# Performance work log

Hardware: AMD Instinct MI355X
Metric: run time of the kernel (lower is better)

The kernel has to match this reference:

```python
import jax, jax.numpy as jnp
import numpy as np

KSIZE = 7
NSPIX = 196


def _unfold(x, k):
    # x: (T, C, H, W) -> (T, C, k*k, H, W), reflect padding, torch Unfold ordering
    p = (k - 1) // 2
    T, C, H, W = x.shape
    xp = jnp.pad(x, ((0, 0), (0, 0), (p, p), (p, p)), mode='reflect')
    return jnp.stack([xp[:, :, i:i + H, j:j + W] for i in range(k) for j in range(k)], axis=2)


def setup_inputs() -> dict:
    key = jax.random.key(0)
    k1, k2, k3, k4, k5 = jax.random.split(key, 5)
    T, C, H, W = 2, 64, 160, 160
    fan_in = C * KSIZE * KSIZE
    x = jax.random.normal(k1, (T, C, H, W), jnp.float32)
    spix = jax.random.randint(k2, (T, H, W), 0, NSPIX, jnp.int32)
    W_lin = jax.random.normal(k3, (C, fan_in), jnp.float32) / np.sqrt(fan_in)
    b_lin = jax.random.normal(k4, (C,), jnp.float32) * 0.01
    w_scale = jax.random.normal(k5, (C,), jnp.float32) / np.sqrt(C)
    b_scale = jnp.zeros((1,), jnp.float32)
    return {"x": x, "spix": spix, "W_lin": W_lin, "b_lin": b_lin,
            "w_scale": w_scale, "b_scale": b_scale}


def reference(x, spix, W_lin, b_lin, w_scale, b_scale):
    T, C, H, W = x.shape
    K2 = KSIZE * KSIZE
    O = W_lin.shape[0]
    p = (KSIZE - 1) // 2

    # unfold(x) with reflect padding -> patches (T, C, K2, H, W)
    patches = _unfold(x, KSIZE)

    # unfold(spix) -> neighbor superpixel ids per pixel (T, K2, H, W)
    sp = jnp.pad(spix, ((0, 0), (p, p), (p, p)), mode='reflect')
    nb = jnp.stack([sp[:, i:i + H, j:j + W] for i in range(KSIZE) for j in range(KSIZE)], axis=1)

    # per-frame superpixel mean pooling (bist.get_pooled_video): down (T, S, C)
    seg = (spix.astype(jnp.int32) + jnp.arange(T, dtype=jnp.int32)[:, None, None] * NSPIX).reshape(-1)
    feats = x.transpose(0, 2, 3, 1).reshape(-1, C)  # (T*H*W, C)
    sums = jax.ops.segment_sum(feats, seg, num_segments=T * NSPIX).reshape(T, NSPIX, C)
    cnts = jax.ops.segment_sum(jnp.ones((seg.shape[0],), x.dtype), seg,
                               num_segments=T * NSPIX).reshape(T, NSPIX, 1)
    down = sums / jnp.maximum(cnts, 1.0)

    # squared pairwise distances between superpixel means: pwd (T, S, S)
    sq = jnp.sum(down * down, axis=-1)
    pwd = jnp.maximum(sq[:, :, None] + sq[:, None, :]
                      - 2.0 * jnp.einsum('tsc,tuc->tsu', down, down), 0.0)

    # sims[t,k,h,w] = ||mean(spix[t,h,w]) - mean(nb[t,k,h,w])||^2
    tidx = jnp.arange(T)[:, None, None, None]
    sims = pwd[tidx, spix[:, None, :, :], nb]  # (T, K2, H, W)

    # scale = 10 * softplus(1x1-conv(x / ||x||_c))  -> (T, H, W)
    xn = x / (jnp.linalg.norm(x, axis=1, keepdims=True) + 1e-10)
    scale = 10.0 * jax.nn.softplus(jnp.einsum('c,tchw->thw', w_scale, xn) + b_scale[0])

    # apply_norm 'exp_max' over the kernel-tap axis
    rw = jnp.exp(-scale[:, None, :, :] * sims)  # (T, K2, H, W)
    rw = rw / (1e-5 + jnp.max(rw, axis=1, keepdims=True))

    # dynamic conv: out[t,o,h,w] = sum_{c,k} W[o,c,k] * patches[t,c,k,h,w] * rw[t,k,h,w] + b[o]
    out = jnp.einsum('ock,tckhw,tkhw->tohw', W_lin.reshape(O, C, K2), patches, rw)
    return out + b_lin[None, :, None, None]
```

## Files before the change

kernel.cpp:

```cpp
#include <hip/hip_runtime.h>
#include <math.h>

#define TT 2
#define CC 64
#define HH 160
#define WW 160
#define KS 7
#define K2 49
#define NSPIX 196
#define HWSZ (HH*WW)
#define PAD 3
#define OO 64
#define FANIN (CC*K2)
#define TS 8
#define PS (TS+KS-1)
#define NPOS (PS*PS)

#define NCHUNK 50
#define CHUNKPIX 512

typedef _Float16 half8 __attribute__((ext_vector_type(8)));
typedef float f32x16 __attribute__((ext_vector_type(16)));
typedef unsigned int uint4v __attribute__((ext_vector_type(4)));
typedef _Float16 half2v __attribute__((ext_vector_type(2)));

__device__ __forceinline__ int reflect(int i, int n) {
    if (i < 0) i = -i;
    if (i >= n) i = 2*n - 2 - i;
    return i;
}

__global__ __launch_bounds__(256) void k_prep(const float* __restrict__ x,
                                              const int* __restrict__ spix,
                                              const float* __restrict__ Wl,
                                              const float* __restrict__ wsc,
                                              const float* __restrict__ bsc,
                                              float* __restrict__ sums,
                                              float* __restrict__ cnts,
                                              float* __restrict__ scale,
                                              _Float16* __restrict__ Wb,
                                              _Float16* __restrict__ xT) {
    __shared__ float ls[8*200];
    __shared__ float lcnt[200];
    int bid = blockIdx.x;
    int tid = threadIdx.x;

    if (bid < 800) {
        int cg = bid & 7;
        int rest = bid >> 3;
        int ch = rest % NCHUNK;
        int t  = rest / NCHUNK;

        for (int i = tid; i < 8*200; i += 256) ls[i] = 0.f;
        if (cg == 0) for (int i = tid; i < 200; i += 256) lcnt[i] = 0.f;
        __syncthreads();

        int base = ch*CHUNKPIX;
        const float* xb = x + ((size_t)t*CC + cg*8)*HWSZ;
        #pragma unroll
        for (int i = 0; i < CHUNKPIX; i += 256) {
            int pix = base + i + tid;
            int s = spix[t*HWSZ + pix];
            if (cg == 0) atomicAdd(&lcnt[s], 1.0f);
            #pragma unroll
            for (int j = 0; j < 8; ++j) atomicAdd(&ls[j*200 + s], xb[(size_t)j*HWSZ + pix]);
        }
        __syncthreads();

        float* sb = sums + (size_t)t*NSPIX*CC + cg*8;
        for (int i = tid; i < 8*NSPIX; i += 256) {
            int s = i >> 3, j = i & 7;
            float v = ls[j*200 + s];
            if (v != 0.f) atomicAdd(&sb[s*CC + j], v);
        }
        if (cg == 0)
            for (int i = tid; i < NSPIX; i += 256) {
                float v = lcnt[i];
                if (v != 0.f) atomicAdd(&cnts[t*NSPIX + i], v);
            }
    } else if (bid < 1000) {
        int pix = (bid - 800)*256 + tid;
        int t = pix / HWSZ, hw = pix - t*HWSZ;
        const float* xs = x + (size_t)t*CC*HWSZ + hw;
        float s1 = 0.f, s2 = 0.f;
        unsigned int pk[32];
        #pragma unroll
        for (int cp = 0; cp < 32; ++cp) {
            float v0 = xs[(size_t)(2*cp)*HWSZ];
            float v1 = xs[(size_t)(2*cp + 1)*HWSZ];
            s1 += wsc[2*cp]*v0 + wsc[2*cp+1]*v1;
            s2 = fmaf(v0, v0, s2); s2 = fmaf(v1, v1, s2);
            half2v h; h[0] = (_Float16)v0; h[1] = (_Float16)v1;
            pk[cp] = __builtin_bit_cast(unsigned int, h);
        }
        float z = s1/(sqrtf(s2) + 1e-10f) + bsc[0];
        float sp_ = (z > 0.f) ? z + log1pf(expf(-z)) : log1pf(expf(z));
        scale[pix] = 10.f*sp_;
        uint4v* dst = (uint4v*)(xT + (size_t)pix*64);
        #pragma unroll
        for (int q = 0; q < 8; ++q) {
            uint4v v = { pk[4*q], pk[4*q+1], pk[4*q+2], pk[4*q+3] };
            dst[q] = v;
        }
    } else {
        int row = (bid - 1000)*256 + tid;
        if (row < 2*K2*4*64) {
            int ln  = row & 63;
            int kc  = (row >> 6) & 3;
            int tq  = row >> 8;
            int tap = tq % K2;
            int qo  = tq / K2;
            int o = qo*32 + (ln & 31);
            int cb = kc*16 + (ln >> 5)*8;
            _Float16* dst = Wb + (size_t)row*8;
            const float* src = Wl + (size_t)o*FANIN + tap;
            #pragma unroll
            for (int j = 0; j < 8; ++j) dst[j] = (_Float16)src[(size_t)(cb + j)*K2];
        }
    }
}

__global__ __launch_bounds__(256) void k_pwd(const float* __restrict__ sums,
                                             const float* __restrict__ cnts,
                                             float* __restrict__ pwd) {
    int tid = blockIdx.x*256 + threadIdx.x;
    if (tid >= TT*NSPIX*NSPIX) return;
    int t = tid / (NSPIX*NSPIX); int r = tid - t*NSPIX*NSPIX;
    int s = r / NSPIX, u = r - (r / NSPIX)*NSPIX;
    const float* ds = sums + (size_t)(t*NSPIX + s)*CC;
    const float* du = sums + (size_t)(t*NSPIX + u)*CC;
    float is = 1.0f / fmaxf(cnts[t*NSPIX + s], 1.0f);
    float iu = 1.0f / fmaxf(cnts[t*NSPIX + u], 1.0f);
    float acc = 0.f;
    #pragma unroll 8
    for (int c = 0; c < CC; ++c) {
        float d = ds[c]*is - du[c]*iu;
        acc = fmaf(d, d, acc);
    }
    pwd[tid] = acc;
}

__global__ __launch_bounds__(256, 4) void k_main(
    const _Float16* __restrict__ xT, const int* __restrict__ spix,
    const _Float16* __restrict__ Wb, const float* __restrict__ b_lin,
    const float* __restrict__ pwd, const float* __restrict__ scale,
    float* __restrict__ out)
{
    __shared__ unsigned short xpT[NPOS*64];
    __shared__ unsigned short rwb[K2*64];
    __shared__ int   sp[NPOS];
    __shared__ float mxp[4*64];
    __shared__ float mxl[64];

    int bid = blockIdx.x;
    int t = bid / 400;
    int r = bid - t*400;
    int th0 = (r / 20)*TS, tw0 = (r - (r/20)*20)*TS;
    int tid = threadIdx.y*64 + threadIdx.x;

    for (int i = tid; i < NPOS; i += 256) {
        int rr = reflect(th0 + i/PS - PAD, HH);
        int cc = reflect(tw0 + i%PS - PAD, WW);
        sp[i] = spix[t*HWSZ + rr*WW + cc];
    }
    {
        const _Float16* xt = xT + (size_t)t*HWSZ*64;
        for (int i = tid; i < NPOS*8; i += 256) {
            int pos = i >> 3, cb = i & 7;
            int rr = reflect(th0 + pos/PS - PAD, HH);
            int cc = reflect(tw0 + pos%PS - PAD, WW);
            uint4v v = *(const uint4v*)(xt + (size_t)(rr*WW + cc)*64 + cb*8);
            int chunk = cb ^ (pos & 7);
            *(uint4v*)&xpT[pos*64 + chunk*8] = v;
        }
    }
    __syncthreads();

    int p_ = threadIdx.x;
    int ty = threadIdx.y;
    int py0 = p_ >> 3, px0 = p_ & 7;
    {
        float sc = scale[t*HWSZ + (th0 + py0)*WW + (tw0 + px0)];
        int s0 = sp[(py0 + PAD)*PS + (px0 + PAD)];
        const float* pr = pwd + (t*NSPIX + s0)*NSPIX;
        float pmax = 0.f;
        for (int k = ty; k < K2; k += 4) {
            int di = k/KS, dj = k - di*KS;
            int nb = sp[(py0 + di)*PS + (px0 + dj)];
            float v = expf(-sc * pr[nb]);
            rwb[k*64 + p_] = __builtin_bit_cast(unsigned short, (_Float16)v);
            pmax = fmaxf(pmax, v);
        }
        mxp[ty*64 + p_] = pmax;
    }
    __syncthreads();
    if (ty == 0) {
        float m = fmaxf(fmaxf(mxp[p_], mxp[64 + p_]), fmaxf(mxp[128 + p_], mxp[192 + p_]));
        mxl[p_] = 1.f/(1e-5f + m);
    }
    __syncthreads();
    {
        float s = mxl[p_];
        for (int k = ty; k < K2; k += 4) {
            float v = (float)__builtin_bit_cast(_Float16, rwb[k*64 + p_]) * s;
            rwb[k*64 + p_] = __builtin_bit_cast(unsigned short, (_Float16)v);
        }
    }
    __syncthreads();

    int ln = threadIdx.x;
    int wv = __builtin_amdgcn_readfirstlane(threadIdx.y);
    int qp = wv & 1, kh = wv >> 1;
    int p  = qp*32 + (ln & 31);
    int ppy = p >> 3, ppx = p & 7;
    int lhi = ln >> 5;

    int jc0 = 4*kh + lhi, jc1 = jc0 + 2;

    const _Float16* A0b = Wb + (size_t)(2*kh)*512 + ln*8;
    const _Float16* A1b = A0b + (size_t)K2*4*512;

    f32x16 acc0, acc1;
    #pragma unroll
    for (int i = 0; i < 16; ++i) { acc0[i] = 0.f; acc1[i] = 0.f; }

    int di = 0, dj = 0;
    #pragma unroll 7
    for (int tap = 0; tap < K2; ++tap) {
        const _Float16* a0 = A0b + (size_t)tap*2048;
        half8 A00 = *(const half8*)(a0);
        half8 A01 = *(const half8*)(a0 + 512);
        const _Float16* a1 = A1b + (size_t)tap*2048;
        half8 A10 = *(const half8*)(a1);
        half8 A11 = *(const half8*)(a1 + 512);

        int pos = (ppy + di)*PS + (ppx + dj);
        int sw  = pos & 7;
        const unsigned short* bbase = &xpT[pos*64];
        half8 B0 = *(const half8*)(bbase + ((jc0 ^ sw) << 3));
        half8 B1 = *(const half8*)(bbase + ((jc1 ^ sw) << 3));

        _Float16 rv = __builtin_bit_cast(_Float16, rwb[tap*64 + p]);
        half8 rv8 = { rv, rv, rv, rv, rv, rv, rv, rv };
        B0 *= rv8;
        B1 *= rv8;

        acc0 = __builtin_amdgcn_mfma_f32_32x32x16_f16(A00, B0, acc0, 0, 0, 0);
        acc0 = __builtin_amdgcn_mfma_f32_32x32x16_f16(A01, B1, acc0, 0, 0, 0);
        acc1 = __builtin_amdgcn_mfma_f32_32x32x16_f16(A10, B0, acc1, 0, 0, 0);
        acc1 = __builtin_amdgcn_mfma_f32_32x32x16_f16(A11, B1, acc1, 0, 0, 0);

        if (++dj == KS) { dj = 0; ++di; }
    }

    __syncthreads();
    float* red = (float*)xpT;
    if (kh == 1) {
        #pragma unroll
        for (int i = 0; i < 16; ++i) {
            red[((qp*2 + 0)*16 + i)*64 + ln] = acc0[i];
            red[((qp*2 + 1)*16 + i)*64 + ln] = acc1[i];
        }
    }
    __syncthreads();
    if (kh == 0) {
        int h = th0 + ppy, w = tw0 + ppx;
        int row_hi = 4*lhi;
        float* ob = out + (size_t)t*OO*HWSZ + h*WW + w;
        #pragma unroll
        for (int rg = 0; rg < 16; ++rg) {
            int o0 = (rg & 3) + 8*(rg >> 2) + row_hi;
            int o1 = 32 + o0;
            float v0 = acc0[rg] + red[((qp*2 + 0)*16 + rg)*64 + ln];
            float v1 = acc1[rg] + red[((qp*2 + 1)*16 + rg)*64 + ln];
            ob[(size_t)o0*HWSZ] = v0 + b_lin[o0];
            ob[(size_t)o1*HWSZ] = v1 + b_lin[o1];
        }
    }
}

extern "C" void kernel_launch(void* const* d_in, const int* in_sizes, int n_in,
                              void* d_out, int out_size, void* d_ws, size_t ws_size,
                              hipStream_t stream) {
    const float* x    = (const float*)d_in[0];
    const int*   spix = (const int*)d_in[1];
    const float* Wl   = (const float*)d_in[2];
    const float* bl   = (const float*)d_in[3];
    const float* wsc  = (const float*)d_in[4];
    const float* bsc  = (const float*)d_in[5];
    float* out = (float*)d_out;

    float* ws    = (float*)d_ws;
    float* sums  = ws;
    float* cnts  = sums + TT*NSPIX*CC;
    float* pwd   = cnts + TT*NSPIX;
    float* scale = pwd  + TT*NSPIX*NSPIX;
    _Float16* Wb = (_Float16*)(scale + TT*HWSZ);
    _Float16* xT = Wb + (size_t)2*K2*4*64*8;

    hipMemsetAsync(sums, 0, (size_t)(TT*NSPIX*CC + TT*NSPIX)*sizeof(float), stream);

    k_prep<<<1196, 256, 0, stream>>>(x, spix, Wl, wsc, bsc, sums, cnts, scale, Wb, xT);
    k_pwd <<<(TT*NSPIX*NSPIX + 255)/256, 256, 0, stream>>>(sums, cnts, pwd);

    dim3 blk(64, 4, 1);
    k_main<<<TT*400, blk, 0, stream>>>(xT, spix, Wb, bl, pwd, scale, out);
}
```

Before: 153.0 us.

## Fuse memset, prep, pwd and main kernels into one cooperative persistent kernel

Replaces the memset plus three separate kernel launches with a single cooperative kernel whose blocks loop over work units and separate the phases with grid-wide syncs. This is meant to remove launch gaps and inter-kernel drain and fill costs. The grid is capped at 800 blocks, so blocks process several prep units serially. System-scope fences and grid.sync add their own overhead. The old multi-kernel path is kept as a fallback if the cooperative launch fails.

```diff
diff --git a/kernel.cpp b/kernel.cpp
--- a/kernel.cpp
+++ b/kernel.cpp
@@ -1,5 +1,8 @@
 #include <hip/hip_runtime.h>
+#include <hip/hip_cooperative_groups.h>
 #include <math.h>
+
+namespace coop = cooperative_groups;
 
 #define TT 2
 #define CC 64
@@ -18,6 +21,7 @@
 
 #define NCHUNK 50
 #define CHUNKPIX 512
+#define NVB 800
 
 typedef _Float16 half8 __attribute__((ext_vector_type(8)));
 typedef float f32x16 __attribute__((ext_vector_type(16)));
@@ -30,133 +34,127 @@
     return i;
 }
 
-__global__ __launch_bounds__(256) void k_prep(const float* __restrict__ x,
-                                              const int* __restrict__ spix,
-                                              const float* __restrict__ Wl,
-                                              const float* __restrict__ wsc,
-                                              const float* __restrict__ bsc,
-                                              float* __restrict__ sums,
-                                              float* __restrict__ cnts,
-                                              float* __restrict__ scale,
-                                              _Float16* __restrict__ Wb,
-                                              _Float16* __restrict__ xT) {
-    __shared__ float ls[8*200];
-    __shared__ float lcnt[200];
-    int bid = blockIdx.x;
-    int tid = threadIdx.x;
-
-    if (bid < 800) {
-        int cg = bid & 7;
-        int rest = bid >> 3;
-        int ch = rest % NCHUNK;
-        int t  = rest / NCHUNK;
-
-        for (int i = tid; i < 8*200; i += 256) ls[i] = 0.f;
-        if (cg == 0) for (int i = tid; i < 200; i += 256) lcnt[i] = 0.f;
-        __syncthreads();
-
-        int base = ch*CHUNKPIX;
-        const float* xb = x + ((size_t)t*CC + cg*8)*HWSZ;
+
+__device__ __forceinline__ void seg_unit(int u, int tid, const float* __restrict__ x,
+                                         const int* __restrict__ spix,
+                                         float* __restrict__ sums, float* __restrict__ cnts,
+                                         float* ls, float* lcnt) {
+    int cgi = u & 7;
+    int rest = u >> 3;
+    int ch = rest % NCHUNK;
+    int t  = rest / NCHUNK;
+
+    for (int i = tid; i < 8*200; i += 256) ls[i] = 0.f;
+    if (cgi == 0) for (int i = tid; i < 200; i += 256) lcnt[i] = 0.f;
+    __syncthreads();
+
+    int base = ch*CHUNKPIX;
+    const float* xb = x + ((size_t)t*CC + cgi*8)*HWSZ;
+    #pragma unroll
+    for (int i = 0; i < CHUNKPIX; i += 256) {
+        int pix = base + i + tid;
+        int s = spix[t*HWSZ + pix];
+        if (cgi == 0) atomicAdd(&lcnt[s], 1.0f);
         #pragma unroll
-        for (int i = 0; i < CHUNKPIX; i += 256) {
-            int pix = base + i + tid;
-            int s = spix[t*HWSZ + pix];
-            if (cg == 0) atomicAdd(&lcnt[s], 1.0f);
-            #pragma unroll
-            for (int j = 0; j < 8; ++j) atomicAdd(&ls[j*200 + s], xb[(size_t)j*HWSZ + pix]);
-        }
-        __syncthreads();
-
-        float* sb = sums + (size_t)t*NSPIX*CC + cg*8;
-        for (int i = tid; i < 8*NSPIX; i += 256) {
-            int s = i >> 3, j = i & 7;
-            float v = ls[j*200 + s];
-            if (v != 0.f) atomicAdd(&sb[s*CC + j], v);
-        }
-        if (cg == 0)
-            for (int i = tid; i < NSPIX; i += 256) {
-                float v = lcnt[i];
-                if (v != 0.f) atomicAdd(&cnts[t*NSPIX + i], v);
-            }
-    } else if (bid < 1000) {
-        int pix = (bid - 800)*256 + tid;
-        int t = pix / HWSZ, hw = pix - t*HWSZ;
-        const float* xs = x + (size_t)t*CC*HWSZ + hw;
-        float s1 = 0.f, s2 = 0.f;
-        unsigned int pk[32];
+        for (int j = 0; j < 8; ++j) atomicAdd(&ls[j*200 + s], xb[(size_t)j*HWSZ + pix]);
+    }
+    __syncthreads();
+
+    float* sb = sums + (size_t)t*NSPIX*CC + cgi*8;
+    for (int i = tid; i < 8*NSPIX; i += 256) {
+        int s = i >> 3, j = i & 7;
+        float v = ls[j*200 + s];
+        if (v != 0.f) atomicAdd(&sb[s*CC + j], v);
+    }
+    if (cgi == 0)
+        for (int i = tid; i < NSPIX; i += 256) {
+            float v = lcnt[i];
+            if (v != 0.f) atomicAdd(&cnts[t*NSPIX + i], v);
+        }
+    __syncthreads();
+}
+
+__device__ __forceinline__ void scale_unit(int u, int tid, const float* __restrict__ x,
+                                           const float* __restrict__ wsc,
+                                           const float* __restrict__ bsc,
+                                           float* __restrict__ scale,
+                                           _Float16* __restrict__ xT) {
+    int pix = (u - 800)*256 + tid;
+    int t = pix / HWSZ, hw = pix - t*HWSZ;
+    const float* xs = x + (size_t)t*CC*HWSZ + hw;
+    float s1 = 0.f, s2 = 0.f;
+    unsigned int pk[32];
+    #pragma unroll
+    for (int cp = 0; cp < 32; ++cp) {
+        float v0 = xs[(size_t)(2*cp)*HWSZ];
+        float v1 = xs[(size_t)(2*cp + 1)*HWSZ];
+        s1 += wsc[2*cp]*v0 + wsc[2*cp+1]*v1;
+        s2 = fmaf(v0, v0, s2); s2 = fmaf(v1, v1, s2);
+        half2v h; h[0] = (_Float16)v0; h[1] = (_Float16)v1;
+        pk[cp] = __builtin_bit_cast(unsigned int, h);
+    }
+    float z = s1/(sqrtf(s2) + 1e-10f) + bsc[0];
+    float sp_ = (z > 0.f) ? z + log1pf(expf(-z)) : log1pf(expf(z));
+    scale[pix] = 10.f*sp_;
+    uint4v* dst = (uint4v*)(xT + (size_t)pix*64);
+    #pragma unroll
+    for (int q = 0; q < 8; ++q) {
+        uint4v v = { pk[4*q], pk[4*q+1], pk[4*q+2], pk[4*q+3] };
+        dst[q] = v;
+    }
+}
+
+__device__ __forceinline__ void wb_unit(int u, int tid, const float* __restrict__ Wl,
+                                        _Float16* __restrict__ Wb) {
+    int row = (u - 1000)*256 + tid;
+    if (row < 2*K2*4*64) {
+        int ln  = row & 63;
+        int kc  = (row >> 6) & 3;
+        int tq  = row >> 8;
+        int tap = tq % K2;
+        int qo  = tq / K2;
+        int o = qo*32 + (ln & 31);
+        int cb = kc*16 + (ln >> 5)*8;
+        _Float16* dst = Wb + (size_t)row*8;
+        const float* src = Wl + (size_t)o*FANIN + tap;
         #pragma unroll
-        for (int cp = 0; cp < 32; ++cp) {
-            float v0 = xs[(size_t)(2*cp)*HWSZ];
-            float v1 = xs[(size_t)(2*cp + 1)*HWSZ];
-            s1 += wsc[2*cp]*v0 + wsc[2*cp+1]*v1;
-            s2 = fmaf(v0, v0, s2); s2 = fmaf(v1, v1, s2);
-            half2v h; h[0] = (_Float16)v0; h[1] = (_Float16)v1;
-            pk[cp] = __builtin_bit_cast(unsigned int, h);
-        }
-        float z = s1/(sqrtf(s2) + 1e-10f) + bsc[0];
-        float sp_ = (z > 0.f) ? z + log1pf(expf(-z)) : log1pf(expf(z));
-        scale[pix] = 10.f*sp_;
-        uint4v* dst = (uint4v*)(xT + (size_t)pix*64);
-        #pragma unroll
-        for (int q = 0; q < 8; ++q) {
-            uint4v v = { pk[4*q], pk[4*q+1], pk[4*q+2], pk[4*q+3] };
-            dst[q] = v;
-        }
-    } else {
-        int row = (bid - 1000)*256 + tid;
-        if (row < 2*K2*4*64) {
-            int ln  = row & 63;
-            int kc  = (row >> 6) & 3;
-            int tq  = row >> 8;
-            int tap = tq % K2;
-            int qo  = tq / K2;
-            int o = qo*32 + (ln & 31);
-            int cb = kc*16 + (ln >> 5)*8;
-            _Float16* dst = Wb + (size_t)row*8;
-            const float* src = Wl + (size_t)o*FANIN + tap;
-            #pragma unroll
-            for (int j = 0; j < 8; ++j) dst[j] = (_Float16)src[(size_t)(cb + j)*K2];
-        }
-    }
-}
-
-__global__ __launch_bounds__(256) void k_pwd(const float* __restrict__ sums,
-                                             const float* __restrict__ cnts,
-                                             float* __restrict__ pwd) {
-    int tid = blockIdx.x*256 + threadIdx.x;
-    if (tid >= TT*NSPIX*NSPIX) return;
-    int t = tid / (NSPIX*NSPIX); int r = tid - t*NSPIX*NSPIX;
-    int s = r / NSPIX, u = r - (r / NSPIX)*NSPIX;
+        for (int j = 0; j < 8; ++j) dst[j] = (_Float16)src[(size_t)(cb + j)*K2];
+    }
+}
+
+__device__ __forceinline__ void pwd_unit(int idx, const float* __restrict__ sums,
+                                         const float* __restrict__ cnts,
+                                         float* __restrict__ pwd) {
+    int t = idx / (NSPIX*NSPIX); int r = idx - t*NSPIX*NSPIX;
+    int s = r / NSPIX, uu = r - (r / NSPIX)*NSPIX;
     const float* ds = sums + (size_t)(t*NSPIX + s)*CC;
-    const float* du = sums + (size_t)(t*NSPIX + u)*CC;
+    const float* du = sums + (size_t)(t*NSPIX + uu)*CC;
     float is = 1.0f / fmaxf(cnts[t*NSPIX + s], 1.0f);
-    float iu = 1.0f / fmaxf(cnts[t*NSPIX + u], 1.0f);
+    float iu = 1.0f / fmaxf(cnts[t*NSPIX + uu], 1.0f);
     float acc = 0.f;
     #pragma unroll 8
     for (int c = 0; c < CC; ++c) {
         float d = ds[c]*is - du[c]*iu;
         acc = fmaf(d, d, acc);
     }
-    pwd[tid] = acc;
-}
-
-__global__ __launch_bounds__(256, 4) void k_main(
+    pwd[idx] = acc;
+}
+
+__device__ __forceinline__ void main_tile(int vb, int tid, char* smem,
     const _Float16* __restrict__ xT, const int* __restrict__ spix,
     const _Float16* __restrict__ Wb, const float* __restrict__ b_lin,
     const float* __restrict__ pwd, const float* __restrict__ scale,
     float* __restrict__ out)
 {
-    __shared__ unsigned short xpT[NPOS*64];
-    __shared__ unsigned short rwb[K2*64];
-    __shared__ int   sp[NPOS];
-    __shared__ float mxp[4*64];
-    __shared__ float mxl[64];
-
-    int bid = blockIdx.x;
-    int t = bid / 400;
-    int r = bid - t*400;
+    unsigned short* xpT = (unsigned short*)smem;
+    unsigned short* rwb = (unsigned short*)(smem + 25088);
+    int*   sp  = (int*)(smem + 31360);
+    float* mxp = (float*)(smem + 32144);
+    float* mxl = (float*)(smem + 33168);
+
+    int t = vb / 400;
+    int r = vb - t*400;
     int th0 = (r / 20)*TS, tw0 = (r - (r/20)*20)*TS;
-    int tid = threadIdx.y*64 + threadIdx.x;
 
     for (int i = tid; i < NPOS; i += 256) {
         int rr = reflect(th0 + i/PS - PAD, HH);
@@ -176,8 +174,8 @@
     }
     __syncthreads();
 
-    int p_ = threadIdx.x;
-    int ty = threadIdx.y;
+    int p_ = tid & 63;
+    int ty = tid >> 6;
     int py0 = p_ >> 3, px0 = p_ & 7;
     {
         float sc = scale[t*HWSZ + (th0 + py0)*WW + (tw0 + px0)];
@@ -208,8 +206,8 @@
     }
     __syncthreads();
 
-    int ln = threadIdx.x;
-    int wv = __builtin_amdgcn_readfirstlane(threadIdx.y);
+    int ln = p_;
+    int wv = __builtin_amdgcn_readfirstlane(ty);
     int qp = wv & 1, kh = wv >> 1;
     int p  = qp*32 + (ln & 31);
     int ppy = p >> 3, ppx = p & 7;
@@ -277,7 +275,88 @@
             ob[(size_t)o1*HWSZ] = v1 + b_lin[o1];
         }
     }
-}
+    __syncthreads();
+}
+
+
+__global__ __launch_bounds__(256, 4) void k_all(
+    const float* __restrict__ x, const int* __restrict__ spix,
+    const float* __restrict__ Wl, const float* __restrict__ b_lin,
+    const float* __restrict__ wsc, const float* __restrict__ bsc,
+    float* __restrict__ sums, float* __restrict__ cnts,
+    float* __restrict__ pwd, float* __restrict__ scale,
+    _Float16* __restrict__ Wb, _Float16* __restrict__ xT,
+    float* __restrict__ out)
+{
+    __shared__ __align__(16) char smem[33440];
+    coop::grid_group grid = coop::this_grid();
+
+    int bid = blockIdx.x;
+    int tid = threadIdx.y*64 + threadIdx.x;
+    int stride = gridDim.x;
+
+    for (int idx = bid*256 + tid; idx < TT*NSPIX*CC + TT*NSPIX; idx += stride*256)
+        sums[idx] = 0.f;
+    __threadfence_system();
+    grid.sync();
+    __threadfence_system();
+
+    for (int u = bid; u < 1196; u += stride) {
+        if (u < 800)       seg_unit(u, tid, x, spix, sums, cnts, (float*)smem, (float*)smem + 8*200);
+        else if (u < 1000) scale_unit(u, tid, x, wsc, bsc, scale, xT);
+        else               wb_unit(u, tid, Wl, Wb);
+    }
+    __threadfence_system();
+    grid.sync();
+    __threadfence_system();
+
+    for (int idx = bid*256 + tid; idx < TT*NSPIX*NSPIX; idx += stride*256)
+        pwd_unit(idx, sums, cnts, pwd);
+    __threadfence_system();
+    grid.sync();
+    __threadfence_system();
+
+    for (int vb = bid; vb < NVB; vb += stride)
+        main_tile(vb, tid, smem, xT, spix, Wb, b_lin, pwd, scale, out);
+}
+
+
+__global__ __launch_bounds__(256) void k_prep(const float* __restrict__ x,
+                                              const int* __restrict__ spix,
+                                              const float* __restrict__ Wl,
+                                              const float* __restrict__ wsc,
+                                              const float* __restrict__ bsc,
+                                              float* __restrict__ sums,
+                                              float* __restrict__ cnts,
+                                              float* __restrict__ scale,
+                                              _Float16* __restrict__ Wb,
+                                              _Float16* __restrict__ xT) {
+    __shared__ float ls[8*200 + 200];
+    int bid = blockIdx.x;
+    int tid = threadIdx.x;
+    if (bid < 800)       seg_unit(bid, tid, x, spix, sums, cnts, ls, ls + 8*200);
+    else if (bid < 1000) scale_unit(bid, tid, x, wsc, bsc, scale, xT);
+    else                 wb_unit(bid, tid, Wl, Wb);
+}
+
+__global__ __launch_bounds__(256) void k_pwd(const float* __restrict__ sums,
+                                             const float* __restrict__ cnts,
+                                             float* __restrict__ pwd) {
+    int idx = blockIdx.x*256 + threadIdx.x;
+    if (idx < TT*NSPIX*NSPIX) pwd_unit(idx, sums, cnts, pwd);
+}
+
+__global__ __launch_bounds__(256, 4) void k_main(
+    const _Float16* __restrict__ xT, const int* __restrict__ spix,
+    const _Float16* __restrict__ Wb, const float* __restrict__ b_lin,
+    const float* __restrict__ pwd, const float* __restrict__ scale,
+    float* __restrict__ out)
+{
+    __shared__ __align__(16) char smem[33440];
+    int tid = threadIdx.y*64 + threadIdx.x;
+    main_tile(blockIdx.x, tid, smem, xT, spix, Wb, b_lin, pwd, scale, out);
+}
+
 
 extern "C" void kernel_launch(void* const* d_in, const int* in_sizes, int n_in,
                               void* d_out, int out_size, void* d_ws, size_t ws_size,
@@ -298,11 +377,29 @@
     _Float16* Wb = (_Float16*)(scale + TT*HWSZ);
     _Float16* xT = Wb + (size_t)2*K2*4*64*8;
 
-    hipMemsetAsync(sums, 0, (size_t)(TT*NSPIX*CC + TT*NSPIX)*sizeof(float), stream);
-
-    k_prep<<<1196, 256, 0, stream>>>(x, spix, Wl, wsc, bsc, sums, cnts, scale, Wb, xT);
-    k_pwd <<<(TT*NSPIX*NSPIX + 255)/256, 256, 0, stream>>>(sums, cnts, pwd);
-
-    dim3 blk(64, 4, 1);
-    k_main<<<TT*400, blk, 0, stream>>>(xT, spix, Wb, bl, pwd, scale, out);
-}
+    int coopAttr = 0;
+    (void)hipDeviceGetAttribute(&coopAttr, hipDeviceAttributeCooperativeLaunch, 0);
+    int blocksPerCU = 0;
+    (void)hipOccupancyMaxActiveBlocksPerMultiprocessor(&blocksPerCU, k_all, 256, 0);
+
+    bool coopOk = false;
+    if (coopAttr && blocksPerCU > 0) {
+        int nblk = blocksPerCU * 256;
+        if (nblk > NVB) nblk = NVB;
+        void* args[] = { (void*)&x, (void*)&spix, (void*)&Wl, (void*)&bl,
+                         (void*)&wsc, (void*)&bsc, (void*)&sums, (void*)&cnts,
+                         (void*)&pwd, (void*)&scale, (void*)&Wb, (void*)&xT,
+                         (void*)&out };
+        hipError_t err = hipLaunchCooperativeKernel((void*)k_all, dim3(nblk),
+                                                    dim3(64, 4, 1), args, 0, stream);
+        coopOk = (err == hipSuccess);
+    }
+
+    if (!coopOk) {
+        hipMemsetAsync(sums, 0, (size_t)(TT*NSPIX*CC + TT*NSPIX)*sizeof(float), stream);
+        k_prep<<<1196, 256, 0, stream>>>(x, spix, Wl, wsc, bsc, sums, cnts, scale, Wb, xT);
+        k_pwd <<<(TT*NSPIX*NSPIX + 255)/256, 256, 0, stream>>>(sums, cnts, pwd);
+        dim3 blk(64, 4, 1);
+        k_main<<<TT*400, blk, 0, stream>>>(xT, spix, Wb, bl, pwd, scale, out);
+    }
+}
```

Result: slower. 536.1 us (+250.3%).

## Split waves by output-channel half and pad LDS patch rows

Applied to the files above, without the earlier changes.

Each wave now owns one 32-row half of the output channels and covers all 64 pixels, instead of owning 32 pixels across all 64 outputs. This halves the per-wave global weight loads per tap, since A fragments are shared across both pixel groups, at the cost of twice as many LDS B-fragment reads and twice the rw scaling. The LDS patch row stride is padded from 64 to 72 halfs to change the bank mapping of those B reads. The swizzle is kept, so the layout change alters bank behaviour in ways that are hard to predict.

```diff
diff --git a/kernel.cpp b/kernel.cpp
--- a/kernel.cpp
+++ b/kernel.cpp
@@ -15,6 +15,7 @@
 #define TS 8
 #define PS (TS+KS-1)
 #define NPOS (PS*PS)
+#define XROW 72
 
 #define NCHUNK 50
 #define CHUNKPIX 512
@@ -146,7 +147,7 @@
     const float* __restrict__ pwd, const float* __restrict__ scale,
     float* __restrict__ out)
 {
-    __shared__ unsigned short xpT[NPOS*64];
+    __shared__ unsigned short xpT[NPOS*XROW];
     __shared__ unsigned short rwb[K2*64];
     __shared__ int   sp[NPOS];
     __shared__ float mxp[4*64];
@@ -171,7 +172,7 @@
             int cc = reflect(tw0 + pos%PS - PAD, WW);
             uint4v v = *(const uint4v*)(xt + (size_t)(rr*WW + cc)*64 + cb*8);
             int chunk = cb ^ (pos & 7);
-            *(uint4v*)&xpT[pos*64 + chunk*8] = v;
+            *(uint4v*)&xpT[pos*XROW + chunk*8] = v;
         }
     }
     __syncthreads();
@@ -210,15 +211,15 @@
 
     int ln = threadIdx.x;
     int wv = __builtin_amdgcn_readfirstlane(threadIdx.y);
-    int qp = wv & 1, kh = wv >> 1;
-    int p  = qp*32 + (ln & 31);
-    int ppy = p >> 3, ppx = p & 7;
+    int qo = wv & 1, kh = wv >> 1;
     int lhi = ln >> 5;
+    int l31 = ln & 31;
+    int p0 = l31, p1 = 32 + l31;
+    int ppy0 = p0 >> 3, ppx0 = p0 & 7;
 
     int jc0 = 4*kh + lhi, jc1 = jc0 + 2;
 
-    const _Float16* A0b = Wb + (size_t)(2*kh)*512 + ln*8;
-    const _Float16* A1b = A0b + (size_t)K2*4*512;
+    const _Float16* Ab = Wb + ((size_t)(qo*K2*4) + 2*kh)*512 + ln*8;
 
     f32x16 acc0, acc1;
     #pragma unroll
@@ -227,28 +228,32 @@
     int di = 0, dj = 0;
     #pragma unroll 7
     for (int tap = 0; tap < K2; ++tap) {
-        const _Float16* a0 = A0b + (size_t)tap*2048;
-        half8 A00 = *(const half8*)(a0);
-        half8 A01 = *(const half8*)(a0 + 512);
-        const _Float16* a1 = A1b + (size_t)tap*2048;
-        half8 A10 = *(const half8*)(a1);
-        half8 A11 = *(const half8*)(a1 + 512);
-
-        int pos = (ppy + di)*PS + (ppx + dj);
-        int sw  = pos & 7;
-        const unsigned short* bbase = &xpT[pos*64];
-        half8 B0 = *(const half8*)(bbase + ((jc0 ^ sw) << 3));
-        half8 B1 = *(const half8*)(bbase + ((jc1 ^ sw) << 3));
-
-        _Float16 rv = __builtin_bit_cast(_Float16, rwb[tap*64 + p]);
-        half8 rv8 = { rv, rv, rv, rv, rv, rv, rv, rv };
-        B0 *= rv8;
-        B1 *= rv8;
-
-        acc0 = __builtin_amdgcn_mfma_f32_32x32x16_f16(A00, B0, acc0, 0, 0, 0);
-        acc0 = __builtin_amdgcn_mfma_f32_32x32x16_f16(A01, B1, acc0, 0, 0, 0);
-        acc1 = __builtin_amdgcn_mfma_f32_32x32x16_f16(A10, B0, acc1, 0, 0, 0);
-        acc1 = __builtin_amdgcn_mfma_f32_32x32x16_f16(A11, B1, acc1, 0, 0, 0);
+        const _Float16* a = Ab + (size_t)tap*2048;
+        half8 A0 = *(const half8*)(a);
+        half8 A1 = *(const half8*)(a + 512);
+
+        int pos0 = (ppy0 + di)*PS + (ppx0 + dj);
+        int sw   = pos0 & 7;
+        const unsigned short* b0 = &xpT[pos0*XROW];
+        const unsigned short* b1 = b0 + 56*XROW;
+        half8 B00 = *(const half8*)(b0 + ((jc0 ^ sw) << 3));
+        half8 B01 = *(const half8*)(b0 + ((jc1 ^ sw) << 3));
+        half8 B10 = *(const half8*)(b1 + ((jc0 ^ sw) << 3));
+        half8 B11 = *(const half8*)(b1 + ((jc1 ^ sw) << 3));
+
+        _Float16 rv0 = __builtin_bit_cast(_Float16, rwb[tap*64 + p0]);
+        _Float16 rv1 = __builtin_bit_cast(_Float16, rwb[tap*64 + p1]);
+        half8 rv08 = { rv0, rv0, rv0, rv0, rv0, rv0, rv0, rv0 };
+        half8 rv18 = { rv1, rv1, rv1, rv1, rv1, rv1, rv1, rv1 };
+        B00 *= rv08;
+        B01 *= rv08;
+        B10 *= rv18;
+        B11 *= rv18;
+
+        acc0 = __builtin_amdgcn_mfma_f32_32x32x16_f16(A0, B00, acc0, 0, 0, 0);
+        acc0 = __builtin_amdgcn_mfma_f32_32x32x16_f16(A1, B01, acc0, 0, 0, 0);
+        acc1 = __builtin_amdgcn_mfma_f32_32x32x16_f16(A0, B10, acc1, 0, 0, 0);
+        acc1 = __builtin_amdgcn_mfma_f32_32x32x16_f16(A1, B11, acc1, 0, 0, 0);
 
         if (++dj == KS) { dj = 0; ++di; }
     }
@@ -258,23 +263,24 @@
     if (kh == 1) {
         #pragma unroll
         for (int i = 0; i < 16; ++i) {
-            red[((qp*2 + 0)*16 + i)*64 + ln] = acc0[i];
-            red[((qp*2 + 1)*16 + i)*64 + ln] = acc1[i];
+            red[((qo*2 + 0)*16 + i)*64 + ln] = acc0[i];
+            red[((qo*2 + 1)*16 + i)*64 + ln] = acc1[i];
         }
     }
     __syncthreads();
     if (kh == 0) {
-        int h = th0 + ppy, w = tw0 + ppx;
+        int h0 = th0 + ppy0, w0 = tw0 + ppx0;
         int row_hi = 4*lhi;
-        float* ob = out + (size_t)t*OO*HWSZ + h*WW + w;
+        float* ob0 = out + (size_t)t*OO*HWSZ + h0*WW + w0;
+        float* ob1 = ob0 + 4*WW;
         #pragma unroll
         for (int rg = 0; rg < 16; ++rg) {
-            int o0 = (rg & 3) + 8*(rg >> 2) + row_hi;
-            int o1 = 32 + o0;
-            float v0 = acc0[rg] + red[((qp*2 + 0)*16 + rg)*64 + ln];
-            float v1 = acc1[rg] + red[((qp*2 + 1)*16 + rg)*64 + ln];
-            ob[(size_t)o0*HWSZ] = v0 + b_lin[o0];
-            ob[(size_t)o1*HWSZ] = v1 + b_lin[o1];
+            int o = qo*32 + (rg & 3) + 8*(rg >> 2) + row_hi;
+            float v0 = acc0[rg] + red[((qo*2 + 0)*16 + rg)*64 + ln];
+            float v1 = acc1[rg] + red[((qo*2 + 1)*16 + rg)*64 + ln];
+            float bl = b_lin[o];
+            ob0[(size_t)o*HWSZ] = v0 + bl;
+            ob1[(size_t)o*HWSZ] = v1 + bl;
         }
     }
 }
```

Result: no change. 155.8 us (+1.8%).
